# Kernel tuning notes

Hardware: AMD Instinct MI355X
Metric: run time of the kernel (lower is better)

## Reference

```python
import jax, jax.numpy as jnp
import numpy as np

B, S, D, H = 256, 128, 1024, 8
DH = D // H  # per-head dim = input_length / head


def setup_inputs() -> dict:
    key = jax.random.key(0)
    ks = jax.random.split(key, 12)
    code = jax.random.normal(ks[0], (B, S, D), dtype=jnp.float32)
    # 0/1 adjacency (PDG relation mask)
    input_relation = jax.random.bernoulli(ks[1], 0.2, (B, S, S)).astype(jnp.float32)
    w = 0.02
    Wq = jax.random.normal(ks[2], (H, D, DH), dtype=jnp.float32) * w
    bq = jnp.zeros((H, DH), dtype=jnp.float32)
    Wk = jax.random.normal(ks[3], (H, D, DH), dtype=jnp.float32) * w
    bk = jnp.zeros((H, DH), dtype=jnp.float32)
    Wv = jax.random.normal(ks[4], (H, D, DH), dtype=jnp.float32) * w
    bv = jnp.zeros((H, DH), dtype=jnp.float32)
    Wo = jax.random.normal(ks[5], (2 * D, D), dtype=jnp.float32) * w
    bo = jnp.zeros((D,), dtype=jnp.float32)
    return {"code": code, "input_relation": input_relation,
            "Wq": Wq, "bq": bq, "Wk": Wk, "bk": bk,
            "Wv": Wv, "bv": bv, "Wo": Wo, "bo": bo}


def reference(code, input_relation, Wq, bq, Wk, bk, Wv, bv, Wo, bo):
    Hn = Wq.shape[0]
    half = Hn // 2
    Sn = code.shape[1]
    E = jnp.eye(Sn, dtype=code.dtype)
    # Faithful to the TF loop: head i < H/2 sees relation + i*I (the loop
    # reassigns input_relation = this_relation + I each iteration);
    # heads i >= H/2 see the ORIGINAL transposed relation.
    i_idx = jnp.arange(half, dtype=code.dtype)  # [half]
    rel_fwd = input_relation[None] + i_idx[:, None, None, None] * E  # [half,B,S,S]
    rel_t = jnp.swapaxes(input_relation, 1, 2)
    rel_bwd = jnp.broadcast_to(rel_t[None], (Hn - half,) + rel_t.shape)
    rels = jnp.concatenate([rel_fwd, rel_bwd], axis=0)  # [H,B,S,S]

    relu = jax.nn.relu
    Q = relu(jnp.einsum('bsd,hdf->hbsf', code, Wq) + bq[:, None, None, :])
    K = relu(jnp.einsum('bsd,hdf->hbsf', code, Wk) + bk[:, None, None, :])
    V = relu(jnp.einsum('bsd,hdf->hbsf', code, Wv) + bv[:, None, None, :])

    attn = jnp.einsum('hbsf,hbtf->hbst', Q, K)  # [H,B,S,S]
    pdg = rels * attn + 1e-11
    # tf.reduce_sum axis=1 (rows) -> our axis=2; axis=2 (cols) -> our axis=3
    indeg = jnp.sqrt(jnp.sum(pdg, axis=2, keepdims=True))   # [H,B,1,S]
    outdeg = jnp.sqrt(jnp.sum(pdg, axis=3, keepdims=True))  # [H,B,S,1]
    pdg = pdg / indeg / outdeg
    softed = rels * pdg
    res = jnp.einsum('hbst,hbtf->hbsf', softed, V)  # [H,B,S,DH]

    # concat heads along features (head 0 first), then concat original code
    all_ch = jnp.transpose(res, (1, 2, 0, 3)).reshape(code.shape[0], Sn, -1)
    add_ori = jnp.concatenate([all_ch, code], axis=-1)  # [B,S,2D]
    out = relu(add_ori @ Wo + bo)
    return out
```

## Files before the change

### kernel.cpp

```cpp
#include <hip/hip_runtime.h>
#include <cstdint>
#include <cstddef>

#define B_  256
#define S_  128
#define D_  1024
#define H_  8
#define DH_ 128
#define M_  (B_ * S_)

typedef _Float16 half8 __attribute__((ext_vector_type(8)));
typedef float    f32x4 __attribute__((ext_vector_type(4)));

#define GLOAD_LDS16(gp, lp)                                                    \
    __builtin_amdgcn_global_load_lds(                                          \
        (const __attribute__((address_space(1))) void*)(gp),                   \
        (__attribute__((address_space(3))) void*)(lp), 16, 0, 0)

__global__ __launch_bounds__(256)
void cvt_code(const float* __restrict__ src, _Float16* __restrict__ dst, int n8)
{
    int i = blockIdx.x * 256 + threadIdx.x;
    if (i >= n8) return;
    const float4* s = (const float4*)src;
    float4 a = s[2 * i], b = s[2 * i + 1];
    half8 o;
    o[0] = (_Float16)a.x; o[1] = (_Float16)a.y; o[2] = (_Float16)a.z; o[3] = (_Float16)a.w;
    o[4] = (_Float16)b.x; o[5] = (_Float16)b.y; o[6] = (_Float16)b.z; o[7] = (_Float16)b.w;
    *(half8*)(dst + (size_t)i * 8) = o;
}

__global__ __launch_bounds__(256)
void cvt_wqkv(const float* __restrict__ Wq, const float* __restrict__ Wk,
              const float* __restrict__ Wv,
              const float* __restrict__ bq, const float* __restrict__ bk,
              const float* __restrict__ bv,
              _Float16* __restrict__ Wt, float* __restrict__ bias_all)
{
    int idx = blockIdx.x * 256 + threadIdx.x;
    if (idx >= 3072 * 128) return;
    int n = idx >> 7, kc = idx & 127, k = kc * 8;
    int qkv = n >> 10, hf = n & 1023, h = hf >> 7, f = hf & 127;
    const float* W = (qkv == 0 ? Wq : (qkv == 1 ? Wk : Wv))
                     + (size_t)h * D_ * DH_ + (size_t)k * DH_ + f;
    half8 o;
    #pragma unroll
    for (int j = 0; j < 8; ++j) o[j] = (_Float16)W[(size_t)j * DH_];
    *(half8*)(Wt + (size_t)n * 1024 + k) = o;
    if (kc == 0)
        bias_all[n] = (qkv == 0 ? bq : (qkv == 1 ? bk : bv))[h * DH_ + f];
}

__global__ __launch_bounds__(256)
void cvt_wo(const float* __restrict__ Wo, _Float16* __restrict__ Wot)
{
    int idx = blockIdx.x * 256 + threadIdx.x;
    if (idx >= 1024 * 256) return;
    int n = idx >> 8, kc = idx & 255, k = kc * 8;
    const float* W = Wo + (size_t)k * 1024 + n;
    half8 o;
    #pragma unroll
    for (int j = 0; j < 8; ++j) o[j] = (_Float16)W[(size_t)j * 1024];
    *(half8*)(Wot + (size_t)n * 2048 + k) = o;
}

template <bool OUTF32>
__global__ __launch_bounds__(512, 1)
void gemm_f16_8p(const _Float16* __restrict__ A1p, const _Float16* __restrict__ A2p,
                 int K1, const _Float16* __restrict__ Bt,
                 const float* __restrict__ bias, void* __restrict__ outp,
                 int Ntot, int Ktot, int ntn)
{
    __shared__ __align__(16) char lds[131072];

    const int tid = threadIdx.x;
    const int w = tid >> 6, l = tid & 63;
    const int wm = w >> 2, wn = w & 3;
    const int lr = l & 15, lg = l >> 4;

    const int cpx = gridDim.x >> 3;
    const int bid = blockIdx.x;
    const int swz = (bid & 7) * cpx + (bid >> 3);
    const int m0 = (swz / ntn) * 256, n0 = (swz % ntn) * 256;

    const int NT = Ktot >> 6;

    const int srow  = l >> 3;
    const int sgcol = ((l & 7) ^ srow) * 8;

    auto stageHalf = [&](int bufi, int t, int half) {
        const int k0 = t << 6;
        const bool isA = (half == 0) || (half == 3);
        const int hh = (half >= 2) ? 1 : 0;
        char* dst0 = lds + bufi * 65536 + (isA ? 0 : 32768) + hh * 16384;
        if (isA) {
            const _Float16* Asrc; int kc;
            if (k0 < K1) { Asrc = A1p; kc = k0; } else { Asrc = A2p; kc = k0 - K1; }
            #pragma unroll
            for (int i = 0; i < 2; ++i) {
                const int c = i * 8 + w;
                const int row = hh * 128 + c * 8 + srow;
                const _Float16* g = Asrc + (size_t)(m0 + row) * 1024 + kc + sgcol;
                GLOAD_LDS16(g, dst0 + c * 1024);
            }
        } else {
            #pragma unroll
            for (int i = 0; i < 2; ++i) {
                const int c = i * 8 + w;
                const int row = hh * 128 + c * 8 + srow;
                const _Float16* g = Bt + (size_t)(n0 + row) * Ktot + k0 + sgcol;
                GLOAD_LDS16(g, dst0 + c * 1024);
            }
        }
    };

    auto ldA = [&](int bufi, int fi, int ks) -> half8 {
        const int row = fi * 32 + wm * 16 + lr;
        const int pos = (ks * 4 + lg) ^ (row & 7);
        return *(const half8*)(lds + bufi * 65536 + row * 128 + pos * 16);
    };
    auto ldB = [&](int bufi, int fj, int ks) -> half8 {
        const int row = fj * 64 + wn * 16 + lr;
        const int pos = (ks * 4 + lg) ^ (row & 7);
        return *(const half8*)(lds + bufi * 65536 + 32768 + row * 128 + pos * 16);
    };

    f32x4 acc[8][4] = {};
    half8 aq[4][2], b0[2][2], b1[2][2];

    stageHalf(0, 0, 0); stageHalf(0, 0, 1); stageHalf(0, 0, 2); stageHalf(0, 0, 3);

    for (int t = 0; t < NT; ++t) {
        const int buf = t & 1;
        const bool nl = (t + 1 < NT);

        asm volatile("s_waitcnt vmcnt(0)" ::: "memory");
        __builtin_amdgcn_s_barrier();

        if (nl) {
            stageHalf(buf ^ 1, t + 1, 0); stageHalf(buf ^ 1, t + 1, 1);
            stageHalf(buf ^ 1, t + 1, 2); stageHalf(buf ^ 1, t + 1, 3);
        }

        #pragma unroll
        for (int fi = 0; fi < 4; ++fi)
            #pragma unroll
            for (int ks = 0; ks < 2; ++ks)
                aq[fi][ks] = ldA(buf, fi, ks);
        #pragma unroll
        for (int fj = 0; fj < 2; ++fj)
            #pragma unroll
            for (int ks = 0; ks < 2; ++ks)
                b0[fj][ks] = ldB(buf, fj, ks);
        #pragma unroll
        for (int fj = 0; fj < 2; ++fj)
            #pragma unroll
            for (int ks = 0; ks < 2; ++ks)
                b1[fj][ks] = ldB(buf, fj + 2, ks);

        __builtin_amdgcn_s_setprio(1);
        #pragma unroll
        for (int ks = 0; ks < 2; ++ks)
            #pragma unroll
            for (int fi = 0; fi < 4; ++fi)
                #pragma unroll
                for (int fj = 0; fj < 2; ++fj)
                    acc[fi][fj] = __builtin_amdgcn_mfma_f32_16x16x32_f16(
                        aq[fi][ks], b0[fj][ks], acc[fi][fj], 0, 0, 0);
        #pragma unroll
        for (int ks = 0; ks < 2; ++ks)
            #pragma unroll
            for (int fi = 0; fi < 4; ++fi)
                #pragma unroll
                for (int fj = 0; fj < 2; ++fj)
                    acc[fi][fj + 2] = __builtin_amdgcn_mfma_f32_16x16x32_f16(
                        aq[fi][ks], b1[fj][ks], acc[fi][fj + 2], 0, 0, 0);
        __builtin_amdgcn_s_setprio(0);

        __builtin_amdgcn_s_barrier();

        #pragma unroll
        for (int fi = 0; fi < 4; ++fi)
            #pragma unroll
            for (int ks = 0; ks < 2; ++ks)
                aq[fi][ks] = ldA(buf, fi + 4, ks);

        __builtin_amdgcn_s_setprio(1);
        #pragma unroll
        for (int ks = 0; ks < 2; ++ks)
            #pragma unroll
            for (int fi = 0; fi < 4; ++fi)
                #pragma unroll
                for (int fj = 0; fj < 2; ++fj)
                    acc[fi + 4][fj + 2] = __builtin_amdgcn_mfma_f32_16x16x32_f16(
                        aq[fi][ks], b1[fj][ks], acc[fi + 4][fj + 2], 0, 0, 0);
        #pragma unroll
        for (int ks = 0; ks < 2; ++ks)
            #pragma unroll
            for (int fi = 0; fi < 4; ++fi)
                #pragma unroll
                for (int fj = 0; fj < 2; ++fj)
                    acc[fi + 4][fj] = __builtin_amdgcn_mfma_f32_16x16x32_f16(
                        aq[fi][ks], b0[fj][ks], acc[fi + 4][fj], 0, 0, 0);
        __builtin_amdgcn_s_setprio(0);
    }

    #pragma unroll
    for (int fi = 0; fi < 8; ++fi) {
        #pragma unroll
        for (int fj = 0; fj < 4; ++fj) {
            const int n = n0 + fj * 64 + wn * 16 + lr;
            const float bs = bias[n];
            #pragma unroll
            for (int rg = 0; rg < 4; ++rg) {
                const int m = m0 + fi * 32 + wm * 16 + lg * 4 + rg;
                float v = acc[fi][fj][rg] + bs;
                v = v > 0.0f ? v : 0.0f;
                if constexpr (OUTF32)
                    ((float*)outp)[(size_t)m * Ntot + n] = v;
                else
                    ((_Float16*)outp)[(size_t)m * Ntot + n] = (_Float16)v;
            }
        }
    }
}

#define PPAD 136
#define VPAD 40

__global__ __launch_bounds__(256, 2)
void attn_pdg_mfma(const _Float16* __restrict__ QKV, const float* __restrict__ Rel,
                   _Float16* __restrict__ resh)
{
    __shared__ __align__(16) char smem[72704];
    _Float16* P     = (_Float16*)smem;
    _Float16* Qs    = (_Float16*)(smem + 34816);
    _Float16* Ks    = Qs + 2 * 4096;
    _Float16* Vt    = (_Float16*)(smem + 34816);
    unsigned* rbits = (unsigned*)(smem + 67584);
    float* rowpart  = (float*)(smem + 69632);
    float* colpart  = (float*)(smem + 70656);
    float* inv_in   = (float*)(smem + 71680);
    float* inv_out  = (float*)(smem + 72192);

    const int tid = threadIdx.x;
    const int w = tid >> 6, l = tid & 63;
    const int wr = w >> 1, wc = w & 1;
    const int lr = l & 15, lg = l >> 4;
    const int b = blockIdx.x, h = blockIdx.y;

    for (int s = w; s < S_; s += 4) {
        const float* row = &Rel[((size_t)b * S_ + s) * S_];
        unsigned long long b0 = __ballot(row[l] > 0.5f);
        unsigned long long b1 = __ballot(row[64 + l] > 0.5f);
        if (l == 0) {
            rbits[s * 4 + 0] = (unsigned)b0; rbits[s * 4 + 1] = (unsigned)(b0 >> 32);
            rbits[s * 4 + 2] = (unsigned)b1; rbits[s * 4 + 3] = (unsigned)(b1 >> 32);
        }
    }

    const size_t gbase = (size_t)(b * S_) * 3072 + h * DH_;

    auto stageQK = [&](int bufi, int t) {
        const int k0 = t * 32;
        const int rr = l >> 2, cc = (l & 3) * 8;
        #pragma unroll
        for (int i = 0; i < 2; ++i) {
            const int row = w * 32 + i * 16;
            const _Float16* gq = QKV + gbase + (size_t)(row + rr) * 3072 + k0 + cc;
            GLOAD_LDS16(gq, Qs + bufi * 4096 + row * 32);
            const _Float16* gk = QKV + gbase + 1024 + (size_t)(row + rr) * 3072 + k0 + cc;
            GLOAD_LDS16(gk, Ks + bufi * 4096 + row * 32);
        }
    };

    f32x4 acc[4][4] = {};
    stageQK(0, 0);
    __syncthreads();
    int buf = 0;
    for (int t = 0; t < 4; ++t) {
        if (t < 3) stageQK(buf ^ 1, t + 1);
        half8 af[4], bf[4];
        #pragma unroll
        for (int i = 0; i < 4; ++i)
            af[i] = *(const half8*)&Qs[buf * 4096 + (wr * 64 + i * 16 + lr) * 32 + lg * 8];
        #pragma unroll
        for (int j = 0; j < 4; ++j)
            bf[j] = *(const half8*)&Ks[buf * 4096 + (wc * 64 + j * 16 + lr) * 32 + lg * 8];
        #pragma unroll
        for (int i = 0; i < 4; ++i)
            #pragma unroll
            for (int j = 0; j < 4; ++j)
                acc[i][j] = __builtin_amdgcn_mfma_f32_16x16x32_f16(af[i], bf[j], acc[i][j], 0, 0, 0);
        __syncthreads();
        buf ^= 1;
    }

    auto relf = [&](int s, int t) -> float {
        float r;
        if (h < H_ / 2) {
            r = (float)((rbits[s * 4 + (t >> 5)] >> (t & 31)) & 1u);
            if (s == t) r += (float)h;
        } else {
            r = (float)((rbits[t * 4 + (s >> 5)] >> (s & 31)) & 1u);
        }
        return r;
    };

    f32x4 p[4][4];
    #pragma unroll
    for (int i = 0; i < 4; ++i)
        #pragma unroll
        for (int j = 0; j < 4; ++j)
            #pragma unroll
            for (int rg = 0; rg < 4; ++rg) {
                const int s = wr * 64 + i * 16 + lg * 4 + rg;
                const int t = wc * 64 + j * 16 + lr;
                p[i][j][rg] = relf(s, t) * acc[i][j][rg] + 1e-11f;
            }

    #pragma unroll
    for (int i = 0; i < 4; ++i)
        #pragma unroll
        for (int rg = 0; rg < 4; ++rg) {
            float part = p[i][0][rg] + p[i][1][rg] + p[i][2][rg] + p[i][3][rg];
            part += __shfl_xor(part, 1);
            part += __shfl_xor(part, 2);
            part += __shfl_xor(part, 4);
            part += __shfl_xor(part, 8);
            if (lr == 0) rowpart[wc * 128 + wr * 64 + i * 16 + lg * 4 + rg] = part;
        }
    #pragma unroll
    for (int j = 0; j < 4; ++j) {
        float part = 0.0f;
        #pragma unroll
        for (int i = 0; i < 4; ++i)
            part += p[i][j][0] + p[i][j][1] + p[i][j][2] + p[i][j][3];
        part += __shfl_xor(part, 16);
        part += __shfl_xor(part, 32);
        if (lg == 0) colpart[wr * 128 + wc * 64 + j * 16 + lr] = part;
    }
    __syncthreads();

    if (tid < 128) {
        inv_in[tid] = rsqrtf(colpart[tid] + colpart[128 + tid]);
    } else {
        const int s = tid - 128;
        inv_out[s] = rsqrtf(rowpart[s] + rowpart[128 + s]);
    }
    __syncthreads();

    float itj[4];
    #pragma unroll
    for (int j = 0; j < 4; ++j) itj[j] = inv_in[wc * 64 + j * 16 + lr];
    #pragma unroll
    for (int i = 0; i < 4; ++i)
        #pragma unroll
        for (int rg = 0; rg < 4; ++rg) {
            const int s = wr * 64 + i * 16 + lg * 4 + rg;
            const float os = inv_out[s];
            #pragma unroll
            for (int j = 0; j < 4; ++j) {
                const int t = wc * 64 + j * 16 + lr;
                const float val = relf(s, t) * p[i][j][rg] * itj[j] * os;
                P[s * PPAD + t] = (_Float16)val;
            }
        }

    const _Float16* Vb = QKV + gbase + 2048;
    uint4 vreg[2];
    auto loadV = [&](int t) {
        #pragma unroll
        for (int ii = 0; ii < 2; ++ii) {
            const int unit = tid + ii * 256;
            const int tt = unit & 31, fg = unit >> 5;
            vreg[ii] = *(const uint4*)&Vb[(size_t)(t * 32 + tt) * 3072 + fg * 8];
        }
    };

    loadV(0);
    f32x4 acc2[4][4] = {};
    for (int t = 0; t < 4; ++t) {
        #pragma unroll
        for (int ii = 0; ii < 2; ++ii) {
            union { uint4 u; _Float16 hh[8]; } uu;
            uu.u = vreg[ii];
            const int unit = tid + ii * 256;
            const int tt = unit & 31, fg = unit >> 5;
            #pragma unroll
            for (int e = 0; e < 8; ++e)
                Vt[(fg * 8 + e) * VPAD + tt] = uu.hh[e];
        }
        __syncthreads();
        if (t < 3) loadV(t + 1);

        half8 af[4], bf[4];
        #pragma unroll
        for (int i = 0; i < 4; ++i)
            af[i] = *(const half8*)&P[(wr * 64 + i * 16 + lr) * PPAD + t * 32 + lg * 8];
        #pragma unroll
        for (int j = 0; j < 4; ++j)
            bf[j] = *(const half8*)&Vt[(wc * 64 + j * 16 + lr) * VPAD + lg * 8];
        #pragma unroll
        for (int i = 0; i < 4; ++i)
            #pragma unroll
            for (int j = 0; j < 4; ++j)
                acc2[i][j] = __builtin_amdgcn_mfma_f32_16x16x32_f16(af[i], bf[j], acc2[i][j], 0, 0, 0);
        __syncthreads();
    }

    #pragma unroll
    for (int i = 0; i < 4; ++i)
        #pragma unroll
        for (int rg = 0; rg < 4; ++rg) {
            const int s = wr * 64 + i * 16 + lg * 4 + rg;
            #pragma unroll
            for (int j = 0; j < 4; ++j) {
                const int f = wc * 64 + j * 16 + lr;
                resh[((size_t)(b * S_ + s)) * 1024 + h * DH_ + f] = (_Float16)acc2[i][j][rg];
            }
        }
}

extern "C" void kernel_launch(void* const* d_in, const int* in_sizes, int n_in,
                              void* d_out, int out_size, void* d_ws, size_t ws_size,
                              hipStream_t stream)
{
    const float* code = (const float*)d_in[0];
    const float* Rel  = (const float*)d_in[1];
    const float* Wq   = (const float*)d_in[2];
    const float* bq   = (const float*)d_in[3];
    const float* Wk   = (const float*)d_in[4];
    const float* bk   = (const float*)d_in[5];
    const float* Wv   = (const float*)d_in[6];
    const float* bv   = (const float*)d_in[7];
    const float* Wo   = (const float*)d_in[8];
    const float* bo   = (const float*)d_in[9];
    float* out = (float*)d_out;
    (void)in_sizes; (void)n_in; (void)out_size; (void)ws_size;

    char* wsp = (char*)d_ws;
    _Float16* codeh = (_Float16*)wsp;  wsp += (size_t)M_ * 1024 * 2;
    _Float16* QKV   = (_Float16*)wsp;  wsp += (size_t)M_ * 3072 * 2;
    _Float16* resh  = (_Float16*)wsp;  wsp += (size_t)M_ * 1024 * 2;
    _Float16* Wt    = (_Float16*)wsp;  wsp += (size_t)3072 * 1024 * 2;
    _Float16* Wot   = (_Float16*)wsp;  wsp += (size_t)1024 * 2048 * 2;
    float* bias_all = (float*)wsp;     wsp += 3072 * 4;

    cvt_code<<<(M_ * 1024 / 8 + 255) / 256, 256, 0, stream>>>(code, codeh, M_ * 1024 / 8);
    cvt_wqkv<<<(3072 * 128 + 255) / 256, 256, 0, stream>>>(Wq, Wk, Wv, bq, bk, bv, Wt, bias_all);
    cvt_wo<<<(1024 * 256 + 255) / 256, 256, 0, stream>>>(Wo, Wot);

    gemm_f16_8p<false><<<(M_ / 256) * (3072 / 256), 512, 0, stream>>>(
        codeh, codeh, 1024, Wt, bias_all, (void*)QKV, 3072, 1024, 3072 / 256);

    attn_pdg_mfma<<<dim3(B_, H_), 256, 0, stream>>>(QKV, Rel, resh);

    gemm_f16_8p<true><<<(M_ / 256) * (1024 / 256), 512, 0, stream>>>(
        resh, codeh, 1024, Wot, bo, (void*)out, 1024, 2048, 1024 / 256);
}
```

Baseline: 576.2 us.

## Stage full Q/K/V tiles into LDS at once with XOR swizzle and reorder grid

The attention kernel now loads the whole 128x128 Q and K tiles into LDS in one shot using an XOR-swizzled layout, replacing the double-buffered 32-column chunks and their per-step barriers. V is prefetched into registers at kernel start and transposed into LDS once, removing the chunked V loop. The grid is reordered so the heads of one batch run in adjacent blocks, which should improve L2 reuse of the relation matrix and QKV rows. LDS use grows slightly and 8 extra uint4 registers stay live across the QK phase, which may pressure occupancy at 2 blocks per CU.

```diff
diff --git a/kernel.cpp b/kernel.cpp
--- a/kernel.cpp
+++ b/kernel.cpp
@@ -225,75 +225,74 @@
     }
 }
 
-#define PPAD 136
-#define VPAD 40
-
 __global__ __launch_bounds__(256, 2)
 void attn_pdg_mfma(const _Float16* __restrict__ QKV, const float* __restrict__ Rel,
                    _Float16* __restrict__ resh)
 {
-    __shared__ __align__(16) char smem[72704];
-    _Float16* P     = (_Float16*)smem;
-    _Float16* Qs    = (_Float16*)(smem + 34816);
-    _Float16* Ks    = Qs + 2 * 4096;
-    _Float16* Vt    = (_Float16*)(smem + 34816);
-    unsigned* rbits = (unsigned*)(smem + 67584);
-    float* rowpart  = (float*)(smem + 69632);
-    float* colpart  = (float*)(smem + 70656);
-    float* inv_in   = (float*)(smem + 71680);
-    float* inv_out  = (float*)(smem + 72192);
+    __shared__ __align__(16) char smem[75776];
+    unsigned* rbits = (unsigned*)(smem + 70656);
+    float* rowpart  = (float*)(smem + 72704);
+    float* colpart  = (float*)(smem + 73728);
+    float* inv_in   = (float*)(smem + 74752);
+    float* inv_out  = (float*)(smem + 75264);
 
     const int tid = threadIdx.x;
     const int w = tid >> 6, l = tid & 63;
     const int wr = w >> 1, wc = w & 1;
     const int lr = l & 15, lg = l >> 4;
-    const int b = blockIdx.x, h = blockIdx.y;
+    const int h = blockIdx.x, b = blockIdx.y;
 
     for (int s = w; s < S_; s += 4) {
         const float* row = &Rel[((size_t)b * S_ + s) * S_];
-        unsigned long long b0 = __ballot(row[l] > 0.5f);
-        unsigned long long b1 = __ballot(row[64 + l] > 0.5f);
+        unsigned long long b0m = __ballot(row[l] > 0.5f);
+        unsigned long long b1m = __ballot(row[64 + l] > 0.5f);
         if (l == 0) {
-            rbits[s * 4 + 0] = (unsigned)b0; rbits[s * 4 + 1] = (unsigned)(b0 >> 32);
-            rbits[s * 4 + 2] = (unsigned)b1; rbits[s * 4 + 3] = (unsigned)(b1 >> 32);
+            rbits[s * 4 + 0] = (unsigned)b0m; rbits[s * 4 + 1] = (unsigned)(b0m >> 32);
+            rbits[s * 4 + 2] = (unsigned)b1m; rbits[s * 4 + 3] = (unsigned)(b1m >> 32);
         }
     }
 
     const size_t gbase = (size_t)(b * S_) * 3072 + h * DH_;
 
-    auto stageQK = [&](int bufi, int t) {
-        const int k0 = t * 32;
-        const int rr = l >> 2, cc = (l & 3) * 8;
-        #pragma unroll
-        for (int i = 0; i < 2; ++i) {
-            const int row = w * 32 + i * 16;
-            const _Float16* gq = QKV + gbase + (size_t)(row + rr) * 3072 + k0 + cc;
-            GLOAD_LDS16(gq, Qs + bufi * 4096 + row * 32);
-            const _Float16* gk = QKV + gbase + 1024 + (size_t)(row + rr) * 3072 + k0 + cc;
-            GLOAD_LDS16(gk, Ks + bufi * 4096 + row * 32);
-        }
-    };
+    const _Float16* Vb = QKV + gbase + 2048;
+    const int vrow = tid >> 1, vcol0 = (tid & 1) * 64;
+    uint4 vreg[8];
+    #pragma unroll
+    for (int j = 0; j < 8; ++j)
+        vreg[j] = *(const uint4*)&Vb[(size_t)vrow * 3072 + vcol0 + j * 8];
+
+    #pragma unroll
+    for (int i = 0; i < 8; ++i) {
+        const int row = (w * 8 + i) * 4 + (l >> 4);
+        const int gsrc = (l & 15) ^ (row & 7);
+        const _Float16* gq = QKV + gbase + (size_t)row * 3072 + gsrc * 8;
+        GLOAD_LDS16(gq, smem + (w * 8 + i) * 1024);
+        const _Float16* gk = QKV + gbase + 1024 + (size_t)row * 3072 + gsrc * 8;
+        GLOAD_LDS16(gk, smem + 32768 + (w * 8 + i) * 1024);
+    }
+    __syncthreads();
 
     f32x4 acc[4][4] = {};
-    stageQK(0, 0);
-    __syncthreads();
-    int buf = 0;
-    for (int t = 0; t < 4; ++t) {
-        if (t < 3) stageQK(buf ^ 1, t + 1);
+    #pragma unroll
+    for (int kc = 0; kc < 4; ++kc) {
         half8 af[4], bf[4];
         #pragma unroll
-        for (int i = 0; i < 4; ++i)
-            af[i] = *(const half8*)&Qs[buf * 4096 + (wr * 64 + i * 16 + lr) * 32 + lg * 8];
-        #pragma unroll
-        for (int j = 0; j < 4; ++j)
-            bf[j] = *(const half8*)&Ks[buf * 4096 + (wc * 64 + j * 16 + lr) * 32 + lg * 8];
+        for (int i = 0; i < 4; ++i) {
+            const int row = wr * 64 + i * 16 + lr;
+            const int pos = (kc * 4 + lg) ^ (row & 7);
+            af[i] = *(const half8*)(smem + row * 256 + pos * 16);
+        }
+        #pragma unroll
+        for (int j = 0; j < 4; ++j) {
+            const int row = wc * 64 + j * 16 + lr;
+            const int pos = (kc * 4 + lg) ^ (row & 7);
+            bf[j] = *(const half8*)(smem + 32768 + row * 256 + pos * 16);
+        }
         #pragma unroll
         for (int i = 0; i < 4; ++i)
             #pragma unroll
             for (int j = 0; j < 4; ++j)
                 acc[i][j] = __builtin_amdgcn_mfma_f32_16x16x32_f16(af[i], bf[j], acc[i][j], 0, 0, 0);
-        __syncthreads();
-        buf ^= 1;
     }
 
     auto relf = [&](int s, int t) -> float {
@@ -363,50 +362,37 @@
             for (int j = 0; j < 4; ++j) {
                 const int t = wc * 64 + j * 16 + lr;
                 const float val = relf(s, t) * p[i][j][rg] * itj[j] * os;
-                P[s * PPAD + t] = (_Float16)val;
-            }
-        }
-
-    const _Float16* Vb = QKV + gbase + 2048;
-    uint4 vreg[2];
-    auto loadV = [&](int t) {
-        #pragma unroll
-        for (int ii = 0; ii < 2; ++ii) {
-            const int unit = tid + ii * 256;
-            const int tt = unit & 31, fg = unit >> 5;
-            vreg[ii] = *(const uint4*)&Vb[(size_t)(t * 32 + tt) * 3072 + fg * 8];
-        }
-    };
-
-    loadV(0);
+                *(_Float16*)(smem + s * 272 + t * 2) = (_Float16)val;
+            }
+        }
+
+    #pragma unroll
+    for (int j = 0; j < 8; ++j) {
+        union { uint4 u; _Float16 hh[8]; } uu;
+        uu.u = vreg[j];
+        #pragma unroll
+        for (int e = 0; e < 8; ++e) {
+            const int f = vcol0 + j * 8 + e;
+            *(_Float16*)(smem + 34816 + f * 280 + vrow * 2) = uu.hh[e];
+        }
+    }
+    __syncthreads();
+
     f32x4 acc2[4][4] = {};
-    for (int t = 0; t < 4; ++t) {
-        #pragma unroll
-        for (int ii = 0; ii < 2; ++ii) {
-            union { uint4 u; _Float16 hh[8]; } uu;
-            uu.u = vreg[ii];
-            const int unit = tid + ii * 256;
-            const int tt = unit & 31, fg = unit >> 5;
-            #pragma unroll
-            for (int e = 0; e < 8; ++e)
-                Vt[(fg * 8 + e) * VPAD + tt] = uu.hh[e];
-        }
-        __syncthreads();
-        if (t < 3) loadV(t + 1);
-
+    #pragma unroll
+    for (int kc = 0; kc < 4; ++kc) {
         half8 af[4], bf[4];
         #pragma unroll
         for (int i = 0; i < 4; ++i)
-            af[i] = *(const half8*)&P[(wr * 64 + i * 16 + lr) * PPAD + t * 32 + lg * 8];
+            af[i] = *(const half8*)(smem + (wr * 64 + i * 16 + lr) * 272 + kc * 64 + lg * 16);
         #pragma unroll
         for (int j = 0; j < 4; ++j)
-            bf[j] = *(const half8*)&Vt[(wc * 64 + j * 16 + lr) * VPAD + lg * 8];
+            bf[j] = *(const half8*)(smem + 34816 + (wc * 64 + j * 16 + lr) * 280 + kc * 64 + lg * 16);
         #pragma unroll
         for (int i = 0; i < 4; ++i)
             #pragma unroll
             for (int j = 0; j < 4; ++j)
                 acc2[i][j] = __builtin_amdgcn_mfma_f32_16x16x32_f16(af[i], bf[j], acc2[i][j], 0, 0, 0);
-        __syncthreads();
     }
 
     #pragma unroll
@@ -454,7 +440,7 @@
     gemm_f16_8p<false><<<(M_ / 256) * (3072 / 256), 512, 0, stream>>>(
         codeh, codeh, 1024, Wt, bias_all, (void*)QKV, 3072, 1024, 3072 / 256);
 
-    attn_pdg_mfma<<<dim3(B_, H_), 256, 0, stream>>>(QKV, Rel, resh);
+    attn_pdg_mfma<<<dim3(H_, B_), 256, 0, stream>>>(QKV, Rel, resh);
 
     gemm_f16_8p<true><<<(M_ / 256) * (1024 / 256), 512, 0, stream>>>(
         resh, codeh, 1024, Wot, bo, (void*)out, 1024, 2048, 1024 / 256);
```

Result: slower. 595.0 us (+3.3%).
